# Performance work log

Measured on AMD Instinct MI355X. Metric: run time of the kernel, lower is better.

Reference implementation:

```python
import jax, jax.numpy as jnp
import numpy as np

B, S, E, H = 4, 8192, 512, 8
D = E // H  # head_dim = 64


def setup_inputs() -> dict:
    key = jax.random.key(0)
    ks = jax.random.split(key, 9)
    scale = 1.0 / np.sqrt(E)
    x = jax.random.normal(ks[0], (B, S, E), dtype=jnp.float32)
    # torch nn.Linear convention: y = x @ W.T + b, W has shape (out, in)
    Wp = jax.random.uniform(ks[1], (E, E), jnp.float32, -scale, scale)
    bp = jax.random.uniform(ks[2], (E,), jnp.float32, -scale, scale)
    Wc = jax.random.uniform(ks[3], (E, E), jnp.float32, -scale, scale)
    bc = jax.random.uniform(ks[4], (E,), jnp.float32, -scale, scale)
    Ws = jax.random.uniform(ks[5], (E, E), jnp.float32, -scale, scale)
    bs = jax.random.uniform(ks[6], (E,), jnp.float32, -scale, scale)
    Wo = jax.random.uniform(ks[7], (E, E), jnp.float32, -scale, scale)
    bo = jax.random.uniform(ks[8], (E,), jnp.float32, -scale, scale)
    return {"x": x, "Wp": Wp, "bp": bp, "Wc": Wc, "bc": bc,
            "Ws": Ws, "bs": bs, "Wo": Wo, "bo": bo}


def reference(x, Wp, bp, Wc, bc, Ws, bs, Wo, bo):
    # Faithful to TreeAttention.forward with tree_structure=None (default path).
    # NOTE: original views projections as (B,S,H,D) without transposing head/seq,
    # so the matmuls mix HEADS per token (HxH scores), not tokens.
    b, s, _ = x.shape
    parent = (jnp.einsum('bse,fe->bsf', x, Wp) + bp).reshape(b, s, H, D)
    child = (jnp.einsum('bse,fe->bsf', x, Wc) + bc).reshape(b, s, H, D)
    sibling = (jnp.einsum('bse,fe->bsf', x, Ws) + bs).reshape(b, s, H, D)
    # per-token head-mixing scores: (B, S, H, H)
    scores = jnp.einsum('bshd,bstd->bsht', parent, child) / jnp.sqrt(
        jnp.asarray(D, dtype=x.dtype))
    attention = jax.nn.softmax(scores, axis=-1)
    # dropout is identity in eval mode (reference runs in inference mode)
    out = jnp.einsum('bsht,bstd->bshd', attention, sibling).reshape(b, s, E)
    return jnp.einsum('bse,fe->bsf', out, Wo) + bo
```

## Files before the change

kernel.cpp:

```cpp
#include <hip/hip_runtime.h>
#include <hip/hip_bf16.h>

typedef unsigned short u16;
typedef __attribute__((ext_vector_type(8))) short bf16x8;
typedef __attribute__((ext_vector_type(4))) float f32x4;
typedef __attribute__((ext_vector_type(8))) unsigned short u16x8;

#define GLDS(gp, lp) __builtin_amdgcn_global_load_lds( \
    (const __attribute__((address_space(1))) void*)(gp), \
    (__attribute__((address_space(3))) void*)(lp), 16, 0, 0)

__device__ __forceinline__ u16 f2b(float f) {
  unsigned u = __builtin_bit_cast(unsigned, f);
  return (u16)((u + 0x7fffu + ((u >> 16) & 1u)) >> 16);
}
__device__ __forceinline__ float b2f(u16 s) {
  return __builtin_bit_cast(float, (unsigned)s << 16);
}

#define BARX() do { __builtin_amdgcn_sched_barrier(0); \
  asm volatile("s_barrier" ::: "memory"); \
  __builtin_amdgcn_sched_barrier(0); } while (0)

__global__ __launch_bounds__(256) void convert_k(
    const float* __restrict__ x, const float* __restrict__ Wp,
    const float* __restrict__ Wc, const float* __restrict__ Ws,
    const float* __restrict__ Wo, u16* __restrict__ xb,
    u16* __restrict__ wall, u16* __restrict__ wob)
{
  const long CX = 2097152;
  const long CW = 98304;
  const long CO = 32768;
  const long total = CX + CW + CO;
  for (long i = (long)blockIdx.x * blockDim.x + threadIdx.x; i < total;
       i += (long)gridDim.x * blockDim.x) {
    const float* src; u16* dst;
    if (i < CX) {
      src = x + i * 8; dst = xb + i * 8;
    } else if (i < CX + CW) {
      long e = (i - CX) * 8;
      int n = (int)(e >> 9), k = (int)(e & 511);
      const float* wr = (n < 512)  ? (Wp + (long)n * 512)
                      : (n < 1024) ? (Wc + (long)(n - 512) * 512)
                                   : (Ws + (long)(n - 1024) * 512);
      src = wr + k; dst = wall + e;
    } else {
      long e = (i - CX - CW) * 8; src = Wo + e; dst = wob + e;
    }
    f32x4 v0 = *(const f32x4*)src;
    f32x4 v1 = *(const f32x4*)(src + 4);
    u16x8 o;
    o[0]=f2b(v0[0]); o[1]=f2b(v0[1]); o[2]=f2b(v0[2]); o[3]=f2b(v0[3]);
    o[4]=f2b(v1[0]); o[5]=f2b(v1[1]); o[6]=f2b(v1[2]); o[7]=f2b(v1[3]);
    *(u16x8*)dst = o;
  }
}

template<int NC, bool BF16OUT>
__global__ __launch_bounds__(512, 2) void gemm8(
    const u16* __restrict__ A, const u16* __restrict__ Bw,
    const float* __restrict__ bias0, const float* __restrict__ bias1,
    const float* __restrict__ bias2, void* __restrict__ Cout)
{
  __shared__ alignas(16) char smem[131072];
  char* sAc = smem;
  char* sBc = smem + 65536;

  const int tid = threadIdx.x;
  const int w = tid >> 6, lane = tid & 63;
  const int wr = w >> 2, wc = w & 3;
  const int ln15 = lane & 15, g4 = lane >> 4, l7 = lane & 7;

  const int nbx = NC / 256;
  const int nwg = nbx * 128;
  const int qq = nwg / 8;
  const int flat = blockIdx.x;
  const int swz = (flat & 7) * qq + (flat >> 3);
  const int bx = swz % nbx, by = swz / nbx;
  const long row0 = (long)by * 256;
  const int col0 = bx * 256;

  const int gsw = (tid & 7) ^ ((tid >> 3) & 7);
  const u16* pA = A + (row0 + (tid >> 3)) * 512 + gsw * 8;
  const u16* pB = Bw + ((long)col0 + (tid >> 3)) * 512 + gsw * 8;

#define STAGE(pp, tt) do { \
    const u16* a0_ = pA + (tt) * 64; const u16* b0_ = pB + (tt) * 64; \
    char* da_ = sAc + (pp) * 32768 + w * 1024; \
    char* db_ = sBc + (pp) * 32768 + w * 1024; \
    GLDS(a0_, da_);          GLDS(a0_ + 32768, da_ + 8192); \
    GLDS(a0_ + 65536, da_ + 16384); GLDS(a0_ + 98304, da_ + 24576); \
    GLDS(b0_, db_);          GLDS(b0_ + 32768, db_ + 8192); \
    GLDS(b0_ + 65536, db_ + 16384); GLDS(b0_ + 98304, db_ + 24576); \
  } while (0)

  const int gkb0 = ((0 + g4) ^ l7) * 16;
  const int gkb1 = ((4 + g4) ^ l7) * 16;
  const int arow = (wr * 128 + ln15) * 128;
  const int brow = (wc * 64 + ln15) * 128;

#define LOAD_A(MH) do { \
    _Pragma("unroll") for (int mf = 0; mf < 4; ++mf) { \
      aF[mf][0] = *(const bf16x8*)(bufA + (MH) * 8192 + mf * 2048 + gkb0); \
      aF[mf][1] = *(const bf16x8*)(bufA + (MH) * 8192 + mf * 2048 + gkb1); \
    } } while (0)
#define LOAD_B(NH, BF) do { \
    _Pragma("unroll") for (int nf = 0; nf < 2; ++nf) { \
      BF[nf][0] = *(const bf16x8*)(bufB + (NH) * 4096 + nf * 2048 + gkb0); \
      BF[nf][1] = *(const bf16x8*)(bufB + (NH) * 4096 + nf * 2048 + gkb1); \
    } } while (0)
#define MFMA_Q(MH, NH, BF) do { \
    _Pragma("unroll") for (int mf = 0; mf < 4; ++mf) \
    _Pragma("unroll") for (int nf = 0; nf < 2; ++nf) { \
      f32x4 c_ = acc[(MH) * 4 + mf][(NH) * 2 + nf]; \
      c_ = __builtin_amdgcn_mfma_f32_16x16x32_bf16(aF[mf][0], BF[nf][0], c_, 0, 0, 0); \
      c_ = __builtin_amdgcn_mfma_f32_16x16x32_bf16(aF[mf][1], BF[nf][1], c_, 0, 0, 0); \
      acc[(MH) * 4 + mf][(NH) * 2 + nf] = c_; \
    } } while (0)

  f32x4 acc[8][4] = {};

  STAGE(0, 0);
  asm volatile("s_waitcnt vmcnt(0)" ::: "memory");
  BARX();

  for (int t = 0; t < 8; ++t) {
    const int p = t & 1;
    const char* bufA = sAc + p * 32768 + arow;
    const char* bufB = sBc + p * 32768 + brow;
    bf16x8 aF[4][2], bFa[2][2], bFb[2][2];

    if (t < 7) STAGE(p ^ 1, t + 1);
    __builtin_amdgcn_sched_barrier(0);

    LOAD_A(0); LOAD_B(0, bFa);
    __builtin_amdgcn_s_setprio(1); MFMA_Q(0, 0, bFa); __builtin_amdgcn_s_setprio(0);
    LOAD_B(1, bFb);
    __builtin_amdgcn_s_setprio(1); MFMA_Q(0, 1, bFb); __builtin_amdgcn_s_setprio(0);
    LOAD_A(1);
    __builtin_amdgcn_s_setprio(1); MFMA_Q(1, 1, bFb); MFMA_Q(1, 0, bFa);
    __builtin_amdgcn_s_setprio(0);

    if (t < 7) {
      asm volatile("s_waitcnt vmcnt(0)" ::: "memory");
      BARX();
    }
  }

  __syncthreads();
  const long rgb = row0 + wr * 128;
  const int cgb = col0 + wc * 64;
  if (BF16OUT) {
    u16* sc = (u16*)(smem + (w << 14));
#pragma unroll
    for (int n = 0; n < 4; ++n) {
      const int colg = cgb + ln15 + n * 16;
      const float* bp_ = (NC == 512) ? bias0
                         : (colg < 512 ? bias0 : (colg < 1024 ? bias1 : bias2));
      const float bv = bp_[colg & 511];
      const int c = ln15 + n * 16;
      const int gsl = c >> 3, co = c & 7;
#pragma unroll
      for (int mi = 0; mi < 8; ++mi)
#pragma unroll
        for (int j = 0; j < 4; ++j) {
          const int r = mi * 16 + (g4 << 2) + j;
          sc[r * 64 + (((gsl ^ (r & 7)) << 3) | co)] = f2b(acc[mi][n][j] + bv);
        }
    }
    asm volatile("s_waitcnt lgkmcnt(0)" ::: "memory");
    __builtin_amdgcn_sched_barrier(0);
#pragma unroll
    for (int it = 0; it < 16; ++it) {
      const int rr = it * 8 + (lane >> 3);
      const int gl = lane & 7;
      u16x8 v = *(const u16x8*)(sc + rr * 64 + ((gl ^ (rr & 7)) << 3));
      *(u16x8*)((u16*)Cout + (rgb + rr) * NC + cgb + gl * 8) = v;
    }
  } else {
    float* scf = (float*)(smem + (w << 14));
#pragma unroll
    for (int h = 0; h < 2; ++h) {
#pragma unroll
      for (int n = 0; n < 4; ++n) {
        const int colg = cgb + ln15 + n * 16;
        const float bv = bias0[colg & 511];
        const int c = ln15 + n * 16;
        const int gsl = c >> 2, co = c & 3;
#pragma unroll
        for (int mf = 0; mf < 4; ++mf)
#pragma unroll
          for (int j = 0; j < 4; ++j) {
            const int r = mf * 16 + (g4 << 2) + j;
            scf[r * 64 + (((gsl ^ (r & 7)) << 2) | co)] = acc[h * 4 + mf][n][j] + bv;
          }
      }
      asm volatile("s_waitcnt lgkmcnt(0)" ::: "memory");
      __builtin_amdgcn_sched_barrier(0);
#pragma unroll
      for (int it = 0; it < 16; ++it) {
        const int rr = it * 4 + (lane >> 4);
        const int gl = lane & 15;
        f32x4 v = *(const f32x4*)(scf + rr * 64 + ((gl ^ (rr & 7)) << 2));
        *(f32x4*)((float*)Cout + (rgb + h * 64 + rr) * NC + cgb + gl * 4) = v;
      }
      asm volatile("s_waitcnt lgkmcnt(0)" ::: "memory");
      __builtin_amdgcn_sched_barrier(0);
    }
  }
#undef STAGE
#undef LOAD_A
#undef LOAD_B
#undef MFMA_Q
}

__global__ __launch_bounds__(256) void attn_k(const u16* __restrict__ PCS,
                                              u16* __restrict__ OUT)
{
  __shared__ float L[4][1664];
  const int w = threadIdx.x >> 6, lane = threadIdx.x & 63;
  const long token = (long)blockIdx.x * 4 + w;
  float* Lw = L[w];
  const int C0 = 544, S0 = 1088, AT0 = 1600;
  const u16* rowp = PCS + token * 1536;
#pragma unroll
  for (int q = 0; q < 3; ++q) {
    u16x8 v = *(const u16x8*)(rowp + q * 512 + lane * 8);
    float* dst = (q < 2) ? (Lw + q * 544 + (lane >> 3) * 68 + (lane & 7) * 8)
                         : (Lw + S0 + lane * 8);
    f32x4 a = {b2f(v[0]), b2f(v[1]), b2f(v[2]), b2f(v[3])};
    f32x4 b = {b2f(v[4]), b2f(v[5]), b2f(v[6]), b2f(v[7])};
    *(f32x4*)dst = a;
    *(f32x4*)(dst + 4) = b;
  }
  const int h = lane >> 3, t = lane & 7;
  float sc = 0.f;
#pragma unroll
  for (int d = 0; d < 64; d += 4) {
    f32x4 pv = *(const f32x4*)(Lw + h * 68 + d);
    f32x4 cv = *(const f32x4*)(Lw + C0 + t * 68 + d);
    sc += pv[0]*cv[0] + pv[1]*cv[1] + pv[2]*cv[2] + pv[3]*cv[3];
  }
  sc *= 0.125f;
  float mx = sc;
  mx = fmaxf(mx, __shfl_xor(mx, 1));
  mx = fmaxf(mx, __shfl_xor(mx, 2));
  mx = fmaxf(mx, __shfl_xor(mx, 4));
  float e = __expf(sc - mx);
  float sm = e;
  sm += __shfl_xor(sm, 1);
  sm += __shfl_xor(sm, 2);
  sm += __shfl_xor(sm, 4);
  Lw[AT0 + lane] = e / sm;
  float o[8] = {0, 0, 0, 0, 0, 0, 0, 0};
#pragma unroll
  for (int tt = 0; tt < 8; ++tt) {
    const float av = Lw[AT0 + h * 8 + tt];
    f32x4 s0 = *(const f32x4*)(Lw + S0 + tt * 64 + t * 8);
    f32x4 s1 = *(const f32x4*)(Lw + S0 + tt * 64 + t * 8 + 4);
    o[0] += av * s0[0]; o[1] += av * s0[1]; o[2] += av * s0[2]; o[3] += av * s0[3];
    o[4] += av * s1[0]; o[5] += av * s1[1]; o[6] += av * s1[2]; o[7] += av * s1[3];
  }
  u16x8 ov;
#pragma unroll
  for (int j = 0; j < 8; ++j) ov[j] = f2b(o[j]);
  *(u16x8*)(OUT + token * 512 + lane * 8) = ov;
}

extern "C" void kernel_launch(void* const* d_in, const int* in_sizes, int n_in,
                              void* d_out, int out_size, void* d_ws, size_t ws_size,
                              hipStream_t stream) {
  const float* x  = (const float*)d_in[0];
  const float* Wp = (const float*)d_in[1];
  const float* bp = (const float*)d_in[2];
  const float* Wc = (const float*)d_in[3];
  const float* bc = (const float*)d_in[4];
  const float* Ws = (const float*)d_in[5];
  const float* bs = (const float*)d_in[6];
  const float* Wo = (const float*)d_in[7];
  const float* bo = (const float*)d_in[8];

  char* ws = (char*)d_ws;
  u16* xb   = (u16*)ws;
  u16* wall = (u16*)(ws + 33554432);
  u16* wob  = (u16*)(ws + 35127296);
  u16* pcs  = (u16*)(ws + 35651584);
  u16* outb = xb;

  convert_k<<<2048, 256, 0, stream>>>(x, Wp, Wc, Ws, Wo, xb, wall, wob);
  gemm8<1536, true><<<768, 512, 0, stream>>>(xb, wall, bp, bc, bs, pcs);
  attn_k<<<8192, 256, 0, stream>>>(pcs, outb);
  gemm8<512, false><<<256, 512, 0, stream>>>(outb, wob, bo, bo, bo, d_out);
}
```

Baseline: 136.5 us.

## Split GEMM staging into half-tile quarters with fine-grained interleaved prefetch

Restructures the GEMM main loop so that global-to-LDS staging is issued in half-tile pieces (A and B halves) spread between the MFMA quarter blocks. Partial vmcnt waits and barriers are placed after each quarter instead of one full wait per K step. The aim is to overlap memory loads with compute more evenly and avoid the stall at the end of each iteration. In exchange there are more barriers per iteration, and the buffer-reuse hazards now depend on carefully chosen vmcnt counts. The LDS layout of the B rows within each half also changes.

```diff
diff --git a/kernel.cpp b/kernel.cpp
--- a/kernel.cpp
+++ b/kernel.cpp
@@ -80,71 +80,95 @@
   const long row0 = (long)by * 256;
   const int col0 = bx * 256;
 
-  const int gsw = (tid & 7) ^ ((tid >> 3) & 7);
-  const u16* pA = A + (row0 + (tid >> 3)) * 512 + gsw * 8;
-  const u16* pB = Bw + ((long)col0 + (tid >> 3)) * 512 + gsw * 8;
-
-#define STAGE(pp, tt) do { \
-    const u16* a0_ = pA + (tt) * 64; const u16* b0_ = pB + (tt) * 64; \
-    char* da_ = sAc + (pp) * 32768 + w * 1024; \
-    char* db_ = sBc + (pp) * 32768 + w * 1024; \
-    GLDS(a0_, da_);          GLDS(a0_ + 32768, da_ + 8192); \
-    GLDS(a0_ + 65536, da_ + 16384); GLDS(a0_ + 98304, da_ + 24576); \
-    GLDS(b0_, db_);          GLDS(b0_ + 32768, db_ + 8192); \
-    GLDS(b0_ + 65536, db_ + 16384); GLDS(b0_ + 98304, db_ + 24576); \
+  const int t8 = tid >> 3;
+  const int gsw = (tid & 7) ^ (t8 & 7);
+  const u16* pA = A + (row0 + t8) * 512 + gsw * 8;
+  const u16* pB = Bw + ((long)col0 + (t8 >> 5) * 64 + (t8 & 31)) * 512 + gsw * 8;
+
+#define STG_A(bb, h, t) do { \
+    const u16* s_ = pA + (h) * 32768 + (t) * 64; \
+    char* d_ = sAc + (bb) * 32768 + (h) * 16384 + w * 1024; \
+    GLDS(s_, d_); GLDS(s_ + 65536, d_ + 8192); \
   } while (0)
-
-  const int gkb0 = ((0 + g4) ^ l7) * 16;
-  const int gkb1 = ((4 + g4) ^ l7) * 16;
-  const int arow = (wr * 128 + ln15) * 128;
-  const int brow = (wc * 64 + ln15) * 128;
-
-#define LOAD_A(MH) do { \
+#define STG_B(bb, h, t) do { \
+    const u16* s_ = pB + (h) * 16384 + (t) * 64; \
+    char* d_ = sBc + (bb) * 32768 + (h) * 16384 + w * 1024; \
+    GLDS(s_, d_); GLDS(s_ + 65536, d_ + 8192); \
+  } while (0)
+
+  const int gkb0 = (g4 ^ l7) << 4;
+  const int gkb1 = ((g4 + 4) ^ l7) << 4;
+  const int aoff = (wr * 64 + ln15) * 128;
+  const int boff = (wc * 32 + ln15) * 128;
+
+#define LOAD_A(bb, MH) do { \
+    const char* ba_ = sAc + (bb) * 32768 + (MH) * 16384 + aoff; \
     _Pragma("unroll") for (int mf = 0; mf < 4; ++mf) { \
-      aF[mf][0] = *(const bf16x8*)(bufA + (MH) * 8192 + mf * 2048 + gkb0); \
-      aF[mf][1] = *(const bf16x8*)(bufA + (MH) * 8192 + mf * 2048 + gkb1); \
+      aF[mf][0] = *(const bf16x8*)(ba_ + mf * 2048 + gkb0); \
+      aF[mf][1] = *(const bf16x8*)(ba_ + mf * 2048 + gkb1); \
     } } while (0)
-#define LOAD_B(NH, BF) do { \
+#define LOAD_B(bb, NH, BF) do { \
+    const char* bb_ = sBc + (bb) * 32768 + (NH) * 16384 + boff; \
     _Pragma("unroll") for (int nf = 0; nf < 2; ++nf) { \
-      BF[nf][0] = *(const bf16x8*)(bufB + (NH) * 4096 + nf * 2048 + gkb0); \
-      BF[nf][1] = *(const bf16x8*)(bufB + (NH) * 4096 + nf * 2048 + gkb1); \
+      BF[nf][0] = *(const bf16x8*)(bb_ + nf * 2048 + gkb0); \
+      BF[nf][1] = *(const bf16x8*)(bb_ + nf * 2048 + gkb1); \
     } } while (0)
 #define MFMA_Q(MH, NH, BF) do { \
+    __builtin_amdgcn_s_setprio(1); \
     _Pragma("unroll") for (int mf = 0; mf < 4; ++mf) \
     _Pragma("unroll") for (int nf = 0; nf < 2; ++nf) { \
       f32x4 c_ = acc[(MH) * 4 + mf][(NH) * 2 + nf]; \
       c_ = __builtin_amdgcn_mfma_f32_16x16x32_bf16(aF[mf][0], BF[nf][0], c_, 0, 0, 0); \
       c_ = __builtin_amdgcn_mfma_f32_16x16x32_bf16(aF[mf][1], BF[nf][1], c_, 0, 0, 0); \
       acc[(MH) * 4 + mf][(NH) * 2 + nf] = c_; \
-    } } while (0)
+    } \
+    __builtin_amdgcn_s_setprio(0); \
+  } while (0)
+#define WAITB(nstr) do { \
+    asm volatile("s_waitcnt vmcnt(" nstr ")" ::: "memory"); BARX(); } while (0)
 
   f32x4 acc[8][4] = {};
 
-  STAGE(0, 0);
-  asm volatile("s_waitcnt vmcnt(0)" ::: "memory");
-  BARX();
-
-  for (int t = 0; t < 8; ++t) {
-    const int p = t & 1;
-    const char* bufA = sAc + p * 32768 + arow;
-    const char* bufB = sBc + p * 32768 + brow;
+  STG_A(0, 0, 0); STG_B(0, 0, 0); STG_B(0, 1, 0); STG_A(0, 1, 0);
+  STG_A(1, 0, 1); STG_B(1, 0, 1); STG_B(1, 1, 1);
+  WAITB("10");
+
+#pragma unroll
+  for (int it = 0; it < 4; ++it) {
+    const int t0 = 2 * it, t1 = t0 + 1;
+    const bool st = (it < 3);
     bf16x8 aF[4][2], bFa[2][2], bFb[2][2];
 
-    if (t < 7) STAGE(p ^ 1, t + 1);
-    __builtin_amdgcn_sched_barrier(0);
-
-    LOAD_A(0); LOAD_B(0, bFa);
-    __builtin_amdgcn_s_setprio(1); MFMA_Q(0, 0, bFa); __builtin_amdgcn_s_setprio(0);
-    LOAD_B(1, bFb);
-    __builtin_amdgcn_s_setprio(1); MFMA_Q(0, 1, bFb); __builtin_amdgcn_s_setprio(0);
-    LOAD_A(1);
-    __builtin_amdgcn_s_setprio(1); MFMA_Q(1, 1, bFb); MFMA_Q(1, 0, bFa);
-    __builtin_amdgcn_s_setprio(0);
-
-    if (t < 7) {
-      asm volatile("s_waitcnt vmcnt(0)" ::: "memory");
-      BARX();
-    }
+    LOAD_A(0, 0); LOAD_B(0, 0, bFa);
+    STG_A(1, 1, t1);
+    MFMA_Q(0, 0, bFa);
+    if (st) WAITB("10"); else WAITB("2");
+    LOAD_B(0, 1, bFb);
+    if (st) STG_A(0, 0, t0 + 2);
+    MFMA_Q(0, 1, bFb);
+    if (st) WAITB("10"); else WAITB("2");
+    LOAD_A(0, 1);
+    if (st) STG_B(0, 0, t0 + 2);
+    MFMA_Q(1, 1, bFb);
+    if (st) WAITB("10"); else WAITB("2");
+    if (st) STG_B(0, 1, t0 + 2);
+    MFMA_Q(1, 0, bFa);
+    if (st) WAITB("10"); else WAITB("2");
+    LOAD_A(1, 0); LOAD_B(1, 0, bFa);
+    if (st) STG_A(0, 1, t0 + 2);
+    MFMA_Q(0, 0, bFa);
+    if (st) WAITB("10"); else WAITB("2");
+    LOAD_B(1, 1, bFb);
+    if (st) STG_A(1, 0, t1 + 2);
+    MFMA_Q(0, 1, bFb);
+    if (st) WAITB("10"); else WAITB("0");
+    LOAD_A(1, 1);
+    if (st) STG_B(1, 0, t1 + 2);
+    MFMA_Q(1, 1, bFb);
+    if (st) WAITB("10"); else WAITB("0");
+    if (st) STG_B(1, 1, t1 + 2);
+    MFMA_Q(1, 0, bFa);
+    if (st) WAITB("10"); else WAITB("0");
   }
 
   __syncthreads();
@@ -208,10 +232,12 @@
       __builtin_amdgcn_sched_barrier(0);
     }
   }
-#undef STAGE
+#undef STG_A
+#undef STG_B
 #undef LOAD_A
 #undef LOAD_B
 #undef MFMA_Q
+#undef WAITB
 }
 
 __global__ __launch_bounds__(256) void attn_k(const u16* __restrict__ PCS,
```

Result: no change. 136.5 us (-0.0%).

## Switch GEMM inner loop from 16x16x32 to 32x32x16 bf16 MFMA

Applied to the files above, without the earlier changes.

Replaces the 16x16x32 MFMA tiling in the bf16 GEMM with 32x32x16 MFMA tiles, so each wave holds a 4x2 grid of 32x32 accumulators. LDS fragment loads are reorganised into four k-steps with double-buffered register fragments, and the epilogue row/column mapping is rewritten for the 32x32 output layout. The larger MFMA shape cuts LDS fragment reads per FLOP and the MFMA issue count. It keeps the same accumulator register footprint but changes the LDS access pattern and swizzle interaction.

```diff
diff --git a/kernel.cpp b/kernel.cpp
--- a/kernel.cpp
+++ b/kernel.cpp
@@ -4,6 +4,7 @@
 typedef unsigned short u16;
 typedef __attribute__((ext_vector_type(8))) short bf16x8;
 typedef __attribute__((ext_vector_type(4))) float f32x4;
+typedef __attribute__((ext_vector_type(16))) float f32x16;
 typedef __attribute__((ext_vector_type(8))) unsigned short u16x8;
 
 #define GLDS(gp, lp) __builtin_amdgcn_global_load_lds( \
@@ -69,7 +70,7 @@
   const int tid = threadIdx.x;
   const int w = tid >> 6, lane = tid & 63;
   const int wr = w >> 2, wc = w & 3;
-  const int ln15 = lane & 15, g4 = lane >> 4, l7 = lane & 7;
+  const int l31 = lane & 31, g1 = lane >> 5, l7 = lane & 7;
 
   const int nbx = NC / 256;
   const int nwg = nbx * 128;
@@ -94,31 +95,29 @@
     GLDS(b0_ + 65536, db_ + 16384); GLDS(b0_ + 98304, db_ + 24576); \
   } while (0)
 
-  const int gkb0 = ((0 + g4) ^ l7) * 16;
-  const int gkb1 = ((4 + g4) ^ l7) * 16;
-  const int arow = (wr * 128 + ln15) * 128;
-  const int brow = (wc * 64 + ln15) * 128;
-
-#define LOAD_A(MH) do { \
-    _Pragma("unroll") for (int mf = 0; mf < 4; ++mf) { \
-      aF[mf][0] = *(const bf16x8*)(bufA + (MH) * 8192 + mf * 2048 + gkb0); \
-      aF[mf][1] = *(const bf16x8*)(bufA + (MH) * 8192 + mf * 2048 + gkb1); \
-    } } while (0)
-#define LOAD_B(NH, BF) do { \
-    _Pragma("unroll") for (int nf = 0; nf < 2; ++nf) { \
-      BF[nf][0] = *(const bf16x8*)(bufB + (NH) * 4096 + nf * 2048 + gkb0); \
-      BF[nf][1] = *(const bf16x8*)(bufB + (NH) * 4096 + nf * 2048 + gkb1); \
-    } } while (0)
-#define MFMA_Q(MH, NH, BF) do { \
-    _Pragma("unroll") for (int mf = 0; mf < 4; ++mf) \
-    _Pragma("unroll") for (int nf = 0; nf < 2; ++nf) { \
-      f32x4 c_ = acc[(MH) * 4 + mf][(NH) * 2 + nf]; \
-      c_ = __builtin_amdgcn_mfma_f32_16x16x32_bf16(aF[mf][0], BF[nf][0], c_, 0, 0, 0); \
-      c_ = __builtin_amdgcn_mfma_f32_16x16x32_bf16(aF[mf][1], BF[nf][1], c_, 0, 0, 0); \
-      acc[(MH) * 4 + mf][(NH) * 2 + nf] = c_; \
-    } } while (0)
-
-  f32x4 acc[8][4] = {};
+  const int arow = (wr * 128 + l31) * 128;
+  const int brow = (wc * 64 + l31) * 128;
+  int kb[4];
+#pragma unroll
+  for (int ks = 0; ks < 4; ++ks) kb[ks] = ((2 * ks + g1) ^ l7) << 4;
+
+#define LOADF(AS, BS, ks) do { \
+    AS[0] = *(const bf16x8*)(bufA + 0 * 4096 + kb[ks]); \
+    AS[1] = *(const bf16x8*)(bufA + 1 * 4096 + kb[ks]); \
+    AS[2] = *(const bf16x8*)(bufA + 2 * 4096 + kb[ks]); \
+    AS[3] = *(const bf16x8*)(bufA + 3 * 4096 + kb[ks]); \
+    BS[0] = *(const bf16x8*)(bufB + 0 * 4096 + kb[ks]); \
+    BS[1] = *(const bf16x8*)(bufB + 1 * 4096 + kb[ks]); \
+  } while (0)
+#define MSTEP(AS, BS) do { \
+    __builtin_amdgcn_s_setprio(1); \
+    _Pragma("unroll") for (int mm = 0; mm < 4; ++mm) \
+    _Pragma("unroll") for (int nn = 0; nn < 2; ++nn) \
+      acc[mm][nn] = __builtin_amdgcn_mfma_f32_32x32x16_bf16(AS[mm], BS[nn], acc[mm][nn], 0, 0, 0); \
+    __builtin_amdgcn_s_setprio(0); \
+  } while (0)
+
+  f32x16 acc[4][2] = {};
 
   STAGE(0, 0);
   asm volatile("s_waitcnt vmcnt(0)" ::: "memory");
@@ -128,18 +127,19 @@
     const int p = t & 1;
     const char* bufA = sAc + p * 32768 + arow;
     const char* bufB = sBc + p * 32768 + brow;
-    bf16x8 aF[4][2], bFa[2][2], bFb[2][2];
+    bf16x8 A0[4], B0[2], A1[4], B1[2];
 
     if (t < 7) STAGE(p ^ 1, t + 1);
     __builtin_amdgcn_sched_barrier(0);
 
-    LOAD_A(0); LOAD_B(0, bFa);
-    __builtin_amdgcn_s_setprio(1); MFMA_Q(0, 0, bFa); __builtin_amdgcn_s_setprio(0);
-    LOAD_B(1, bFb);
-    __builtin_amdgcn_s_setprio(1); MFMA_Q(0, 1, bFb); __builtin_amdgcn_s_setprio(0);
-    LOAD_A(1);
-    __builtin_amdgcn_s_setprio(1); MFMA_Q(1, 1, bFb); MFMA_Q(1, 0, bFa);
-    __builtin_amdgcn_s_setprio(0);
+    LOADF(A0, B0, 0);
+    LOADF(A1, B1, 1);
+    MSTEP(A0, B0);
+    LOADF(A0, B0, 2);
+    MSTEP(A1, B1);
+    LOADF(A1, B1, 3);
+    MSTEP(A0, B0);
+    MSTEP(A1, B1);
 
     if (t < 7) {
       asm volatile("s_waitcnt vmcnt(0)" ::: "memory");
@@ -153,19 +153,19 @@
   if (BF16OUT) {
     u16* sc = (u16*)(smem + (w << 14));
 #pragma unroll
-    for (int n = 0; n < 4; ++n) {
-      const int colg = cgb + ln15 + n * 16;
+    for (int nn = 0; nn < 2; ++nn) {
+      const int c = nn * 32 + l31;
+      const int colg = cgb + c;
       const float* bp_ = (NC == 512) ? bias0
                          : (colg < 512 ? bias0 : (colg < 1024 ? bias1 : bias2));
       const float bv = bp_[colg & 511];
-      const int c = ln15 + n * 16;
       const int gsl = c >> 3, co = c & 7;
 #pragma unroll
-      for (int mi = 0; mi < 8; ++mi)
-#pragma unroll
-        for (int j = 0; j < 4; ++j) {
-          const int r = mi * 16 + (g4 << 2) + j;
-          sc[r * 64 + (((gsl ^ (r & 7)) << 3) | co)] = f2b(acc[mi][n][j] + bv);
+      for (int mm = 0; mm < 4; ++mm)
+#pragma unroll
+        for (int r = 0; r < 16; ++r) {
+          const int row = mm * 32 + (r & 3) + 8 * (r >> 2) + 4 * g1;
+          sc[row * 64 + (((gsl ^ (row & 7)) << 3) | co)] = f2b(acc[mm][nn][r] + bv);
         }
     }
     asm volatile("s_waitcnt lgkmcnt(0)" ::: "memory");
@@ -182,17 +182,17 @@
 #pragma unroll
     for (int h = 0; h < 2; ++h) {
 #pragma unroll
-      for (int n = 0; n < 4; ++n) {
-        const int colg = cgb + ln15 + n * 16;
+      for (int nn = 0; nn < 2; ++nn) {
+        const int c = nn * 32 + l31;
+        const int colg = cgb + c;
         const float bv = bias0[colg & 511];
-        const int c = ln15 + n * 16;
         const int gsl = c >> 2, co = c & 3;
 #pragma unroll
-        for (int mf = 0; mf < 4; ++mf)
-#pragma unroll
-          for (int j = 0; j < 4; ++j) {
-            const int r = mf * 16 + (g4 << 2) + j;
-            scf[r * 64 + (((gsl ^ (r & 7)) << 2) | co)] = acc[h * 4 + mf][n][j] + bv;
+        for (int mh = 0; mh < 2; ++mh)
+#pragma unroll
+          for (int r = 0; r < 16; ++r) {
+            const int row = mh * 32 + (r & 3) + 8 * (r >> 2) + 4 * g1;
+            scf[row * 64 + (((gsl ^ (row & 7)) << 2) | co)] = acc[h * 2 + mh][nn][r] + bv;
           }
       }
       asm volatile("s_waitcnt lgkmcnt(0)" ::: "memory");
@@ -209,9 +209,8 @@
     }
   }
 #undef STAGE
-#undef LOAD_A
-#undef LOAD_B
-#undef MFMA_Q
+#undef LOADF
+#undef MSTEP
 }
 
 __global__ __launch_bounds__(256) void attn_k(const u16* __restrict__ PCS,
```

New measurement: 143.1 us. 1.05x slower.
